# Kernel optimization log

Measured on AMD Instinct MI355X. Metric: run time of the kernel, lower is better.

## Reference

```python
import jax, jax.numpy as jnp
import numpy as np

N = 100000   # nodes
E = 3200000  # edges (before self-loops)
IN, H, OUT = 128, 256, 40

def glorot(key, shape):
    lim = (6.0 / (shape[0] + shape[1])) ** 0.5
    return jax.random.uniform(key, shape, jnp.float32, -lim, lim)

def setup_inputs() -> dict:
    key = jax.random.key(0)
    ks = jax.random.split(key, 8)
    x = jax.random.normal(ks[0], (N, IN), jnp.float32)
    edge_index = jax.random.randint(ks[1], (2, E), 0, N, dtype=jnp.int32)
    return {
        "x": x,
        "edge_index": edge_index,
        "W0": glorot(ks[2], (IN, H)),  "b0": jnp.zeros((H,), jnp.float32),
        "W1": glorot(ks[3], (H, H)),   "b1": jnp.zeros((H,), jnp.float32),
        "W2": glorot(ks[4], (H, OUT)), "b2": jnp.zeros((OUT,), jnp.float32),
    }

def _gcn_norm(edge_index, n):
    # PyG gcn_norm: add self-loops, symmetric D^{-1/2} A D^{-1/2}
    loops = jnp.arange(n, dtype=edge_index.dtype)
    src = jnp.concatenate([edge_index[0], loops])
    dst = jnp.concatenate([edge_index[1], loops])
    deg = jax.ops.segment_sum(jnp.ones_like(src, jnp.float32), dst, num_segments=n)
    dinv = jnp.where(deg > 0, jax.lax.rsqrt(deg), 0.0)
    norm = dinv[src] * dinv[dst]  # [E+N]
    return src, dst, norm

def _gcn_layer(h, W, b, src, dst, norm, n):
    h = h @ W                                   # transform first (PyG order)
    msg = h[src] * norm[:, None]                # gather + scale
    agg = jax.ops.segment_sum(msg, dst, num_segments=n)  # scatter-add
    return agg + b

def reference(x, edge_index, W0, b0, W1, b1, W2, b2):
    n = x.shape[0]
    src, dst, norm = _gcn_norm(edge_index, n)
    h = jnp.tanh(_gcn_layer(x, W0, b0, src, dst, norm, n))  # dropout = identity (eval)
    h = jnp.tanh(_gcn_layer(h, W1, b1, src, dst, norm, n))
    out = _gcn_layer(h, W2, b2, src, dst, norm, n)
    return jax.nn.log_softmax(out, axis=1)
```

## Files before the change

### kernel.cpp

```cpp
#include <hip/hip_runtime.h>
#include <hip/hip_bf16.h>
#include <cmath>


typedef unsigned short u16;
typedef __attribute__((ext_vector_type(8))) short short8;
typedef __attribute__((ext_vector_type(4))) float f32x4;

#define BSHIFT 10
#define BNODES (1 << BSHIFT)
#define ECAP   36864
#define BMASK 0x00FF00FFu

__device__ __forceinline__ u16 f2bf(float f) {
    unsigned int u = __float_as_uint(f);
    u += 0x7fffu + ((u >> 16) & 1u);
    return (u16)(u >> 16);
}

__device__ __forceinline__ int q8(float v) {
    return (int)rintf(fminf(fmaxf(v, -127.0f), 127.0f));
}


__global__ __launch_bounds__(128) void init_gcur_kernel(
        int* __restrict__ gcur, int nb) {
    int b = blockIdx.x * 128 + threadIdx.x;
    if (b < nb) gcur[b] = b * ECAP;
}

__global__ __launch_bounds__(256) void bucketize_kernel(
        const int* __restrict__ src, const int* __restrict__ dst,
        int* __restrict__ gcur, unsigned int* __restrict__ ebuf, int E) {
    __shared__ int cnt[128];
    __shared__ int base[128];
    int tid = threadIdx.x;
    int chunk0 = blockIdx.x * 8192;
    int cend = min(chunk0 + 8192, E);
    for (int r0 = chunk0; r0 < cend; r0 += 2048) {
        if (tid < 128) cnt[tid] = 0;
        __syncthreads();
        int rank[8], bk[8];
        unsigned int pk[8];
#pragma unroll
        for (int j = 0; j < 8; j++) {
            int e = r0 + j * 256 + tid;
            bk[j] = -1;
            if (e < cend) {
                int d = dst[e];
                bk[j] = d >> BSHIFT;
                pk[j] = (unsigned int)src[e] | ((unsigned int)(d & (BNODES - 1)) << 17);
                rank[j] = atomicAdd(&cnt[bk[j]], 1);
            }
        }
        __syncthreads();
        if (tid < 128 && cnt[tid] > 0) base[tid] = atomicAdd(&gcur[tid], cnt[tid]);
        __syncthreads();
#pragma unroll
        for (int j = 0; j < 8; j++)
            if (bk[j] >= 0) ebuf[base[bk[j]] + rank[j]] = pk[j];
        __syncthreads();
    }
}

__global__ __launch_bounds__(256) void bucket_csr_kernel(
        const unsigned int* __restrict__ ebuf, const int* __restrict__ gcur,
        int* __restrict__ degi, float* __restrict__ dinv,
        int* __restrict__ rs, int* __restrict__ csr, int N) {
    __shared__ int h[BNODES];
    __shared__ int lp[BNODES];
    __shared__ int ps[256];
    int b = blockIdx.x;
    int t = threadIdx.x;
    int nb0 = b << BSHIFT;
    int nodes = min(BNODES, N - nb0);

    int acc = 0;
    for (int j = t; j < b; j += 256) acc += gcur[j] - j * ECAP;
    ps[t] = acc;
    __syncthreads();
    for (int off = 128; off; off >>= 1) {
        if (t < off) ps[t] += ps[t + off];
        __syncthreads();
    }
    int bbase = ps[0];
    __syncthreads();

    for (int i = t; i < BNODES; i += 256) h[i] = 0;
    __syncthreads();
    int estart = b * ECAP;
    int eend = gcur[b];
    for (int e = estart + t; e < eend; e += 256)
        atomicAdd(&h[ebuf[e] >> 17], 1);
    __syncthreads();

    int a0 = h[t * 4], a1 = h[t * 4 + 1], a2 = h[t * 4 + 2], a3 = h[t * 4 + 3];
    int tsum = a0 + a1 + a2 + a3;
    ps[t] = tsum;
    __syncthreads();
    for (int off = 1; off < 256; off <<= 1) {
        int u = (t >= off) ? ps[t - off] : 0;
        __syncthreads();
        ps[t] += u;
        __syncthreads();
    }
    int texcl = ps[t] - tsum;
    lp[t * 4]     = texcl;
    lp[t * 4 + 1] = texcl + a0;
    lp[t * 4 + 2] = texcl + a0 + a1;
    lp[t * 4 + 3] = texcl + a0 + a1 + a2;
    __syncthreads();

    for (int i = t; i < nodes; i += 256) {
        int d = h[i];
        degi[nb0 + i] = d;
        dinv[nb0 + i] = rsqrtf((float)d + 1.0f);
        rs[nb0 + i] = bbase + lp[i];
    }
    __syncthreads();
    for (int i = t; i < BNODES; i += 256) h[i] = bbase + lp[i];
    __syncthreads();

    for (int e = estart + t; e < eend; e += 256) {
        unsigned int v = ebuf[e];
        int s = v & 0x1FFFF;
        int dl = v >> 17;
        int pos = atomicAdd(&h[dl], 1);
        csr[pos] = s;
    }
}

__global__ __launch_bounds__(256) void wt_all_kernel(
        const float* __restrict__ W0, const float* __restrict__ W1,
        const float* __restrict__ W2, u16* __restrict__ Wt0,
        u16* __restrict__ Wt1, u16* __restrict__ Wt2) {
    int i = blockIdx.x * 256 + threadIdx.x;
    if (i < 32768) {
        int k = i >> 8, c = i & 255;
        Wt0[c * 128 + k] = f2bf(W0[i]);
    } else if (i < 98304) {
        int j = i - 32768;
        int k = j >> 8, c = j & 255;
        Wt1[c * 256 + k] = f2bf(W1[j]);
    } else if (i < 108544) {
        int j = i - 98304;
        int k = j / 40, c = j - k * 40;
        Wt2[c * 256 + k] = f2bf(W2[j]);
    }
}

__global__ __launch_bounds__(256) void scale_x_kernel(
        const float* __restrict__ x, const float* __restrict__ dinv,
        unsigned int* __restrict__ out, int total4) {
    int i = blockIdx.x * 256 + threadIdx.x;
    if (i >= total4) return;
    int n = i >> 5;
    float4 v = reinterpret_cast<const float4*>(x)[i];
    float s = dinv[n] * 63.5f;
    int a0 = q8(v.x * s), a1 = q8(v.y * s), a2 = q8(v.z * s), a3 = q8(v.w * s);
    out[i] = (unsigned int)(a0 & 0xff) | ((unsigned int)(a1 & 0xff) << 8) |
             ((unsigned int)(a2 & 0xff) << 16) | ((unsigned int)(a3 & 0xff) << 24);
}

#define ACC8(q0, q1)                                                  \
    do {                                                              \
        aex += (q0) & BMASK; aox += ((q0) >> 8) & BMASK;              \
        aey += (q1) & BMASK; aoy += ((q1) >> 8) & BMASK;              \
    } while (0)

__global__ __launch_bounds__(256) void agg128_i8_kernel(
        const signed char* __restrict__ in, u16* __restrict__ out,
        const int* __restrict__ rs, const int* __restrict__ deg,
        const int* __restrict__ csr, const float* __restrict__ dinv, int n) {
    int wid = blockIdx.x * 4 + (threadIdx.x >> 6);
    if (wid >= n) return;
    int lane = threadIdx.x & 63;
    int quad = lane >> 4;
    int l16 = lane & 15;
    int start = rs[wid];
    int cnt = deg[wid];

    unsigned int aex = 0, aox = 0, aey = 0, aoy = 0;
    if (quad == 0) {
        uint2 q = *reinterpret_cast<const uint2*>(
            in + (size_t)wid * 128 + l16 * 8);
        q.x ^= 0x80808080u; q.y ^= 0x80808080u;
        ACC8(q.x, q.y);
    }
    int i = 0;
    for (; i + 16 <= cnt; i += 16) {
        int s[4];
#pragma unroll
        for (int j = 0; j < 4; j++) s[j] = csr[start + i + 4 * j + quad];
#pragma unroll
        for (int j = 0; j < 4; j++) {
            uint2 q = *reinterpret_cast<const uint2*>(
                in + (size_t)s[j] * 128 + l16 * 8);
            q.x ^= 0x80808080u; q.y ^= 0x80808080u;
            ACC8(q.x, q.y);
        }
    }
    for (; i + 4 <= cnt; i += 4) {
        int s0 = csr[start + i + quad];
        uint2 q = *reinterpret_cast<const uint2*>(
            in + (size_t)s0 * 128 + l16 * 8);
        q.x ^= 0x80808080u; q.y ^= 0x80808080u;
        ACC8(q.x, q.y);
    }
    int rem = cnt - i;
    if (quad < rem) {
        int s0 = csr[start + i + quad];
        uint2 q = *reinterpret_cast<const uint2*>(
            in + (size_t)s0 * 128 + l16 * 8);
        q.x ^= 0x80808080u; q.y ^= 0x80808080u;
        ACC8(q.x, q.y);
    }
    aex += (unsigned int)__shfl((int)aex, lane + 32);
    aox += (unsigned int)__shfl((int)aox, lane + 32);
    aey += (unsigned int)__shfl((int)aey, lane + 32);
    aoy += (unsigned int)__shfl((int)aoy, lane + 32);
    aex += (unsigned int)__shfl((int)aex, lane + 16);
    aox += (unsigned int)__shfl((int)aox, lane + 16);
    aey += (unsigned int)__shfl((int)aey, lane + 16);
    aoy += (unsigned int)__shfl((int)aoy, lane + 16);
    if (lane < 16) {
        int T = cnt + 1;
        int bias = 128 * T;
        float c = dinv[wid] * (2.0f / 127.0f);
        float f0 = (float)((int)(aex & 0xFFFFu) - bias) * c;
        float f1 = (float)((int)(aox & 0xFFFFu) - bias) * c;
        float f2 = (float)((int)(aex >> 16) - bias) * c;
        float f3 = (float)((int)(aox >> 16) - bias) * c;
        float f4 = (float)((int)(aey & 0xFFFFu) - bias) * c;
        float f5 = (float)((int)(aoy & 0xFFFFu) - bias) * c;
        float f6 = (float)((int)(aey >> 16) - bias) * c;
        float f7 = (float)((int)(aoy >> 16) - bias) * c;
        uint4 o;
        o.x = (unsigned)f2bf(f0) | ((unsigned)f2bf(f1) << 16);
        o.y = (unsigned)f2bf(f2) | ((unsigned)f2bf(f3) << 16);
        o.z = (unsigned)f2bf(f4) | ((unsigned)f2bf(f5) << 16);
        o.w = (unsigned)f2bf(f6) | ((unsigned)f2bf(f7) << 16);
        reinterpret_cast<uint4*>(out + (size_t)wid * 128)[l16] = o;
    }
}

__global__ __launch_bounds__(256) void agg_i8_kernel(
        const signed char* __restrict__ in, u16* __restrict__ out,
        const int* __restrict__ rs, const int* __restrict__ deg,
        const int* __restrict__ csr, const float* __restrict__ dinv, int n) {
    int wid = blockIdx.x * 4 + (threadIdx.x >> 6);
    if (wid >= n) return;
    int lane = threadIdx.x & 63;
    int start = rs[wid];
    int cnt = deg[wid];

    unsigned int q = *reinterpret_cast<const unsigned int*>(
        in + (size_t)wid * 256 + lane * 4) ^ 0x80808080u;
    unsigned int ae = q & BMASK, ao = (q >> 8) & BMASK;

    int i = 0;
    for (; i + 16 <= cnt; i += 16) {
        int s[16];
#pragma unroll
        for (int j = 0; j < 16; j++)
            s[j] = __builtin_amdgcn_readfirstlane(csr[start + i + j]);
        unsigned int qq[16];
#pragma unroll
        for (int j = 0; j < 16; j++)
            qq[j] = *reinterpret_cast<const unsigned int*>(
                in + (size_t)s[j] * 256 + lane * 4);
#pragma unroll
        for (int j = 0; j < 16; j++) {
            unsigned int v = qq[j] ^ 0x80808080u;
            ae += v & BMASK;
            ao += (v >> 8) & BMASK;
        }
    }
    if (i < cnt) {
        int s[16];
#pragma unroll
        for (int j = 0; j < 16; j++) {
            int e = i + j;
            e = (e < cnt) ? e : (cnt - 1);
            s[j] = __builtin_amdgcn_readfirstlane(csr[start + e]);
        }
        unsigned int qq[16];
#pragma unroll
        for (int j = 0; j < 16; j++)
            qq[j] = *reinterpret_cast<const unsigned int*>(
                in + (size_t)s[j] * 256 + lane * 4);
#pragma unroll
        for (int j = 0; j < 16; j++) {
            unsigned int m = (i + j < cnt) ? 0xFFFFFFFFu : 0u;
            unsigned int v = (qq[j] ^ 0x80808080u) & m;
            ae += v & BMASK;
            ao += (v >> 8) & BMASK;
        }
    }

    int bias = 128 * (cnt + 1);
    float c = dinv[wid] * (1.0f / 127.0f);
    float f0 = (float)((int)(ae & 0xFFFFu) - bias) * c;
    float f1 = (float)((int)(ao & 0xFFFFu) - bias) * c;
    float f2 = (float)((int)(ae >> 16) - bias) * c;
    float f3 = (float)((int)(ao >> 16) - bias) * c;
    uint2 o;
    o.x = (unsigned)f2bf(f0) | ((unsigned)f2bf(f1) << 16);
    o.y = (unsigned)f2bf(f2) | ((unsigned)f2bf(f3) << 16);
    reinterpret_cast<uint2*>(out + (size_t)wid * 256)[lane] = o;
}

template<int EPI, typename CT>
__global__ __launch_bounds__(256) void mfma_mm_kernel(
        const u16* __restrict__ A, const u16* __restrict__ Bt,
        CT* __restrict__ C, int M, int K, int NC,
        const float* __restrict__ bias, const float* __restrict__ postscale,
        float qs) {
    __shared__ u16 As[128 * 40];
    __shared__ u16 Bs[64 * 40];
    int t = threadIdx.x;
    int w = t >> 6, lane = t & 63, quad = lane >> 4, l16 = lane & 15;
    int row0 = blockIdx.x * 128;
    int col0 = blockIdx.y * 64;

    f32x4 acc[2][4];
#pragma unroll
    for (int s = 0; s < 2; s++)
#pragma unroll
        for (int nb = 0; nb < 4; nb++)
            acc[s][nb] = (f32x4){0.f, 0.f, 0.f, 0.f};

    int bn = t >> 2, bkq = (t & 3) << 3;
    for (int k0 = 0; k0 < K; k0 += 32) {
#pragma unroll
        for (int i = t; i < 512; i += 256) {
            int r = i >> 2, c = (i & 3) << 3;
            int gr = row0 + r;
            uint4 v = {0u, 0u, 0u, 0u};
            if (gr < M)
                v = *reinterpret_cast<const uint4*>(A + (size_t)gr * K + k0 + c);
            *reinterpret_cast<uint4*>(&As[r * 40 + c]) = v;
        }
        {
            int gc = col0 + bn;
            uint4 v = {0u, 0u, 0u, 0u};
            if (gc < NC)
                v = *reinterpret_cast<const uint4*>(Bt + (size_t)gc * K + k0 + bkq);
            *reinterpret_cast<uint4*>(&Bs[bn * 40 + bkq]) = v;
        }
        __syncthreads();

        short8 af[2], bf[4];
        af[0] = *reinterpret_cast<const short8*>(&As[(w * 32 + l16) * 40 + quad * 8]);
        af[1] = *reinterpret_cast<const short8*>(&As[(w * 32 + 16 + l16) * 40 + quad * 8]);
#pragma unroll
        for (int nb = 0; nb < 4; nb++)
            bf[nb] = *reinterpret_cast<const short8*>(&Bs[(nb * 16 + l16) * 40 + quad * 8]);
#pragma unroll
        for (int s = 0; s < 2; s++)
#pragma unroll
            for (int nb = 0; nb < 4; nb++)
                acc[s][nb] = __builtin_amdgcn_mfma_f32_16x16x32_bf16(
                    af[s], bf[nb], acc[s][nb], 0, 0, 0);
        __syncthreads();
    }

#pragma unroll
    for (int s = 0; s < 2; s++) {
        int rbase = row0 + w * 32 + s * 16 + quad * 4;
#pragma unroll
        for (int nb = 0; nb < 4; nb++) {
            int gc = col0 + nb * 16 + l16;
#pragma unroll
            for (int r = 0; r < 4; r++) {
                int gr = rbase + r;
                if (gr >= M || gc >= NC) continue;
                float v = acc[s][nb][r];
                if constexpr (EPI == 1) v = tanhf(v + bias[gc]);
                else                    v = v * postscale[gr];
                if constexpr (sizeof(CT) == 1) {
                    float m = qs;
                    if constexpr (EPI == 1) m *= postscale[gr];
                    C[(size_t)gr * NC + gc] = (CT)q8(v * m);
                } else {
                    C[(size_t)gr * NC + gc] = (CT)f2bf(v);
                }
            }
        }
    }
}

__global__ __launch_bounds__(256) void agg40_ls_kernel(
        const signed char* __restrict__ in, const int* __restrict__ rs,
        const int* __restrict__ deg, const int* __restrict__ csr,
        const float* __restrict__ dinv, const float* __restrict__ bias,
        float* __restrict__ out, int n) {
    int wid = blockIdx.x * 4 + (threadIdx.x >> 6);
    if (wid >= n) return;
    int lane = threadIdx.x & 63;
    int grp = lane / 5;
    int l5 = lane - grp * 5;
    bool act = lane < 60;
    int start = rs[wid];
    int cnt = deg[wid];

    unsigned int aex = 0, aox = 0, aey = 0, aoy = 0;
    if (lane < 5) {
        uint2 q = *reinterpret_cast<const uint2*>(
            in + (size_t)wid * 40 + l5 * 8);
        q.x ^= 0x80808080u; q.y ^= 0x80808080u;
        ACC8(q.x, q.y);
    }
    for (int base = 0; base < cnt; base += 12) {
        int e = base + grp;
        if (act && e < cnt) {
            int s0 = csr[start + e];
            uint2 q = *reinterpret_cast<const uint2*>(
                in + (size_t)s0 * 40 + l5 * 8);
            q.x ^= 0x80808080u; q.y ^= 0x80808080u;
            ACC8(q.x, q.y);
        }
    }
    aex += (unsigned int)__shfl((int)aex, lane + 30);
    aox += (unsigned int)__shfl((int)aox, lane + 30);
    aey += (unsigned int)__shfl((int)aey, lane + 30);
    aoy += (unsigned int)__shfl((int)aoy, lane + 30);
    aex += (unsigned int)__shfl((int)aex, lane + 15);
    aox += (unsigned int)__shfl((int)aox, lane + 15);
    aey += (unsigned int)__shfl((int)aey, lane + 15);
    aoy += (unsigned int)__shfl((int)aoy, lane + 15);
    aex += (unsigned int)__shfl((int)aex, lane + 5) + (unsigned int)__shfl((int)aex, lane + 10);
    aox += (unsigned int)__shfl((int)aox, lane + 5) + (unsigned int)__shfl((int)aox, lane + 10);
    aey += (unsigned int)__shfl((int)aey, lane + 5) + (unsigned int)__shfl((int)aey, lane + 10);
    aoy += (unsigned int)__shfl((int)aoy, lane + 5) + (unsigned int)__shfl((int)aoy, lane + 10);

    bool act5 = lane < 5;
    float s = dinv[wid];
    float v0 = -INFINITY, v1 = -INFINITY, v2 = -INFINITY, v3 = -INFINITY;
    float v4 = -INFINITY, v5 = -INFINITY, v6 = -INFINITY, v7 = -INFINITY;
    if (act5) {
        int bb = 128 * (cnt + 1);
        float c = s * (1.0f / 63.0f);
        int cc = lane * 8;
        v0 = (float)((int)(aex & 0xFFFFu) - bb) * c + bias[cc + 0];
        v1 = (float)((int)(aox & 0xFFFFu) - bb) * c + bias[cc + 1];
        v2 = (float)((int)(aex >> 16) - bb) * c + bias[cc + 2];
        v3 = (float)((int)(aox >> 16) - bb) * c + bias[cc + 3];
        v4 = (float)((int)(aey & 0xFFFFu) - bb) * c + bias[cc + 4];
        v5 = (float)((int)(aoy & 0xFFFFu) - bb) * c + bias[cc + 5];
        v6 = (float)((int)(aey >> 16) - bb) * c + bias[cc + 6];
        v7 = (float)((int)(aoy >> 16) - bb) * c + bias[cc + 7];
    }
    float m = fmaxf(fmaxf(fmaxf(v0, v1), fmaxf(v2, v3)),
                    fmaxf(fmaxf(v4, v5), fmaxf(v6, v7)));
    for (int off = 4; off; off >>= 1) m = fmaxf(m, __shfl_xor(m, off));
    float e = 0.f;
    if (act5) e = __expf(v0 - m) + __expf(v1 - m) + __expf(v2 - m) + __expf(v3 - m)
                + __expf(v4 - m) + __expf(v5 - m) + __expf(v6 - m) + __expf(v7 - m);
    for (int off = 4; off; off >>= 1) e += __shfl_xor(e, off);
    float ls = logf(e);
    if (act5) {
        float4 o0, o1;
        o0.x = v0 - m - ls; o0.y = v1 - m - ls; o0.z = v2 - m - ls; o0.w = v3 - m - ls;
        o1.x = v4 - m - ls; o1.y = v5 - m - ls; o1.z = v6 - m - ls; o1.w = v7 - m - ls;
        float4* op = reinterpret_cast<float4*>(out + (size_t)wid * 40 + lane * 8);
        op[0] = o0;
        op[1] = o1;
    }
}

extern "C" void kernel_launch(void* const* d_in, const int* in_sizes, int n_in,
                              void* d_out, int out_size, void* d_ws, size_t ws_size,
                              hipStream_t stream) {
    const float* x  = (const float*)d_in[0];
    const int*   ei = (const int*)d_in[1];
    const float* W0 = (const float*)d_in[2];
    const float* b0 = (const float*)d_in[3];
    const float* W1 = (const float*)d_in[4];
    const float* b1 = (const float*)d_in[5];
    const float* W2 = (const float*)d_in[6];
    const float* b2 = (const float*)d_in[7];
    float* out = (float*)d_out;

    const int N = in_sizes[0] / 128;
    const int E = in_sizes[1] / 2;
    const int IN = 128, H = 256, OUT = 40;
    const int NB = (N + BNODES - 1) >> BSHIFT;

    char* p = (char*)d_ws;
    auto carve = [&](size_t bytes) -> void* {
        void* r = (void*)p;
        p += (bytes + 255) & ~(size_t)255;
        return r;
    };
    float*        dinv = (float*)carve((size_t)N * 4);
    int*          degi = (int*)  carve((size_t)N * 4);
    int*          rs   = (int*)  carve((size_t)N * 4);
    int*          gcur = (int*)  carve((size_t)128 * 4);
    int*          csr  = (int*)  carve((size_t)E * 4);
    unsigned int* ebuf = (unsigned int*)carve((size_t)NB * ECAP * 4);
    u16*          Wt0  = (u16*)  carve((size_t)IN * H * 2);
    u16*          Wt1  = (u16*)  carve((size_t)H * H * 2);
    u16*          Wt2  = (u16*)  carve((size_t)H * OUT * 2);
    u16*          U1   = (u16*)  carve((size_t)N * H * 2);
    u16*          U2   = (u16*)  carve((size_t)N * H * 2);

    signed char* Xq   = (signed char*)U1;
    u16*         T0bf = U1 + (size_t)N * IN / 2 + 64;
    signed char* H0q  = (signed char*)U2;
    u16*         T1bf = U1;
    u16*         h1bf = U2;
    signed char* G2q  = (signed char*)U1;

    const int* src = ei;
    const int* dst = ei + E;

    int gW = (N + 3) / 4;
    int gMM = (N + 127) / 128;
    int gA = (E + 8191) / 8192;

    init_gcur_kernel<<<1, 128, 0, stream>>>(gcur, NB);
    bucketize_kernel<<<gA, 256, 0, stream>>>(src, dst, gcur, ebuf, E);
    bucket_csr_kernel<<<NB, 256, 0, stream>>>(
        ebuf, gcur, degi, dinv, rs, csr, N);

    wt_all_kernel<<<(108544 + 255) / 256, 256, 0, stream>>>(
        W0, W1, W2, Wt0, Wt1, Wt2);

    int t4x = N * (IN / 4);
    scale_x_kernel<<<(t4x + 255) / 256, 256, 0, stream>>>(
        x, dinv, (unsigned int*)Xq, t4x);
    agg128_i8_kernel<<<gW, 256, 0, stream>>>(Xq, T0bf, rs, degi, csr, dinv, N);
    mfma_mm_kernel<1, signed char><<<dim3(gMM, H / 64), 256, 0, stream>>>(
        T0bf, Wt0, H0q, N, IN, H, b0, dinv, 127.0f);

    agg_i8_kernel<<<gW, 256, 0, stream>>>(H0q, T1bf, rs, degi, csr, dinv, N);
    mfma_mm_kernel<1, u16><<<dim3(gMM, H / 64), 256, 0, stream>>>(
        T1bf, Wt1, h1bf, N, H, H, b1, nullptr, 0.f);

    mfma_mm_kernel<0, signed char><<<dim3(gMM, 1), 256, 0, stream>>>(
        h1bf, Wt2, G2q, N, H, OUT, nullptr, dinv, 63.0f);
    agg40_ls_kernel<<<gW, 256, 0, stream>>>(G2q, rs, degi, csr, dinv, b2, out, N);
}
```

Before: 605.5 us.

## Quantize layer-1 output to int8 and pad layer-2 features to 64-byte rows

Layer 1's tanh output is now stored as int8 instead of bf16. A new dedicated MFMA kernel consumes it, dequantizing int8 to bf16 in shared memory and computing the 40-column projection, then writes int8 rows padded to a 64-byte stride. The final aggregation/log-softmax kernel is reworked to use 4 lanes x 16 bytes per edge with 16 edges per iteration and power-of-two shuffle reductions, replacing the awkward 5-lane grouping. This cuts the memory traffic of the intermediate activation and aligns gathers, at the cost of extra quantization error and padded storage.

```diff
diff --git a/kernel.cpp b/kernel.cpp
--- a/kernel.cpp
+++ b/kernel.cpp
@@ -380,11 +380,93 @@
                 else                    v = v * postscale[gr];
                 if constexpr (sizeof(CT) == 1) {
                     float m = qs;
-                    if constexpr (EPI == 1) m *= postscale[gr];
+                    if constexpr (EPI == 1) { if (postscale) m *= postscale[gr]; }
                     C[(size_t)gr * NC + gc] = (CT)q8(v * m);
                 } else {
                     C[(size_t)gr * NC + gc] = (CT)f2bf(v);
                 }
+            }
+        }
+    }
+}
+
+__global__ __launch_bounds__(256) void mfma_mm2_i8_kernel(
+        const signed char* __restrict__ A, const u16* __restrict__ Bt,
+        signed char* __restrict__ C, int M, const float* __restrict__ postscale) {
+    __shared__ u16 As[128 * 40];
+    __shared__ u16 Bs[48 * 40];
+    int t = threadIdx.x;
+    int w = t >> 6, lane = t & 63, quad = lane >> 4, l16 = lane & 15;
+    int row0 = blockIdx.x * 128;
+
+    f32x4 acc[2][3];
+#pragma unroll
+    for (int s = 0; s < 2; s++)
+#pragma unroll
+        for (int nb = 0; nb < 3; nb++)
+            acc[s][nb] = (f32x4){0.f, 0.f, 0.f, 0.f};
+
+    int ar = t >> 1, aoff = (t & 1) << 4;
+    for (int k0 = 0; k0 < 256; k0 += 32) {
+        {
+            int gr = row0 + ar;
+            uint4 v = {0u, 0u, 0u, 0u};
+            if (gr < M)
+                v = *reinterpret_cast<const uint4*>(A + (size_t)gr * 256 + k0 + aoff);
+            unsigned int wds[8];
+#pragma unroll
+            for (int u = 0; u < 4; u++) {
+                unsigned int q = (&v.x)[u];
+                float g0 = (float)(int)(signed char)(q & 0xffu);
+                float g1 = (float)(int)(signed char)((q >> 8) & 0xffu);
+                float g2 = (float)(int)(signed char)((q >> 16) & 0xffu);
+                float g3 = (float)(int)(signed char)(q >> 24);
+                wds[u * 2]     = (unsigned)f2bf(g0) | ((unsigned)f2bf(g1) << 16);
+                wds[u * 2 + 1] = (unsigned)f2bf(g2) | ((unsigned)f2bf(g3) << 16);
+            }
+            uint4 o0 = {wds[0], wds[1], wds[2], wds[3]};
+            uint4 o1 = {wds[4], wds[5], wds[6], wds[7]};
+            *reinterpret_cast<uint4*>(&As[ar * 40 + aoff]) = o0;
+            *reinterpret_cast<uint4*>(&As[ar * 40 + aoff + 8]) = o1;
+        }
+        if (t < 192) {
+            int gc = t >> 2, kq = (t & 3) << 3;
+            uint4 v = {0u, 0u, 0u, 0u};
+            if (gc < 40)
+                v = *reinterpret_cast<const uint4*>(Bt + (size_t)gc * 256 + k0 + kq);
+            *reinterpret_cast<uint4*>(&Bs[gc * 40 + kq]) = v;
+        }
+        __syncthreads();
+
+        short8 af[2], bf[3];
+        af[0] = *reinterpret_cast<const short8*>(&As[(w * 32 + l16) * 40 + quad * 8]);
+        af[1] = *reinterpret_cast<const short8*>(&As[(w * 32 + 16 + l16) * 40 + quad * 8]);
+#pragma unroll
+        for (int nb = 0; nb < 3; nb++)
+            bf[nb] = *reinterpret_cast<const short8*>(&Bs[(nb * 16 + l16) * 40 + quad * 8]);
+#pragma unroll
+        for (int s = 0; s < 2; s++)
+#pragma unroll
+            for (int nb = 0; nb < 3; nb++)
+                acc[s][nb] = __builtin_amdgcn_mfma_f32_16x16x32_bf16(
+                    af[s], bf[nb], acc[s][nb], 0, 0, 0);
+        __syncthreads();
+    }
+
+    const float QS = 63.0f / 127.0f;
+#pragma unroll
+    for (int s = 0; s < 2; s++) {
+        int rbase = row0 + w * 32 + s * 16 + quad * 4;
+#pragma unroll
+        for (int nb = 0; nb < 3; nb++) {
+            int gc = nb * 16 + l16;
+            if (gc >= 40) continue;
+#pragma unroll
+            for (int r = 0; r < 4; r++) {
+                int gr = rbase + r;
+                if (gr >= M) continue;
+                float v = acc[s][nb][r] * postscale[gr] * QS;
+                C[(size_t)gr * 64 + gc] = (signed char)q8(v);
             }
         }
     }
@@ -398,74 +480,79 @@
     int wid = blockIdx.x * 4 + (threadIdx.x >> 6);
     if (wid >= n) return;
     int lane = threadIdx.x & 63;
-    int grp = lane / 5;
-    int l5 = lane - grp * 5;
-    bool act = lane < 60;
+    int grp = lane >> 2;
+    int l4 = lane & 3;
     int start = rs[wid];
     int cnt = deg[wid];
 
-    unsigned int aex = 0, aox = 0, aey = 0, aoy = 0;
-    if (lane < 5) {
-        uint2 q = *reinterpret_cast<const uint2*>(
-            in + (size_t)wid * 40 + l5 * 8);
-        q.x ^= 0x80808080u; q.y ^= 0x80808080u;
-        ACC8(q.x, q.y);
-    }
-    for (int base = 0; base < cnt; base += 12) {
+    unsigned int a0 = 0, a1 = 0, a2 = 0, a3 = 0, a4 = 0, a5 = 0, a6 = 0, a7 = 0;
+#define ACCR(q)                                                        \
+    do {                                                               \
+        unsigned int x = (q).x ^ 0x80808080u, y = (q).y ^ 0x80808080u, \
+                     z = (q).z ^ 0x80808080u, w = (q).w ^ 0x80808080u; \
+        a0 += x & BMASK; a1 += (x >> 8) & BMASK;                       \
+        a2 += y & BMASK; a3 += (y >> 8) & BMASK;                       \
+        a4 += z & BMASK; a5 += (z >> 8) & BMASK;                       \
+        a6 += w & BMASK; a7 += (w >> 8) & BMASK;                       \
+    } while (0)
+
+    if (grp == 0) {
+        uint4 q = *reinterpret_cast<const uint4*>(in + (size_t)wid * 64 + l4 * 16);
+        ACCR(q);
+    }
+    for (int base = 0; base < cnt; base += 16) {
         int e = base + grp;
-        if (act && e < cnt) {
+        if (e < cnt) {
             int s0 = csr[start + e];
-            uint2 q = *reinterpret_cast<const uint2*>(
-                in + (size_t)s0 * 40 + l5 * 8);
-            q.x ^= 0x80808080u; q.y ^= 0x80808080u;
-            ACC8(q.x, q.y);
-        }
-    }
-    aex += (unsigned int)__shfl((int)aex, lane + 30);
-    aox += (unsigned int)__shfl((int)aox, lane + 30);
-    aey += (unsigned int)__shfl((int)aey, lane + 30);
-    aoy += (unsigned int)__shfl((int)aoy, lane + 30);
-    aex += (unsigned int)__shfl((int)aex, lane + 15);
-    aox += (unsigned int)__shfl((int)aox, lane + 15);
-    aey += (unsigned int)__shfl((int)aey, lane + 15);
-    aoy += (unsigned int)__shfl((int)aoy, lane + 15);
-    aex += (unsigned int)__shfl((int)aex, lane + 5) + (unsigned int)__shfl((int)aex, lane + 10);
-    aox += (unsigned int)__shfl((int)aox, lane + 5) + (unsigned int)__shfl((int)aox, lane + 10);
-    aey += (unsigned int)__shfl((int)aey, lane + 5) + (unsigned int)__shfl((int)aey, lane + 10);
-    aoy += (unsigned int)__shfl((int)aoy, lane + 5) + (unsigned int)__shfl((int)aoy, lane + 10);
-
-    bool act5 = lane < 5;
-    float s = dinv[wid];
-    float v0 = -INFINITY, v1 = -INFINITY, v2 = -INFINITY, v3 = -INFINITY;
-    float v4 = -INFINITY, v5 = -INFINITY, v6 = -INFINITY, v7 = -INFINITY;
-    if (act5) {
+            uint4 q = *reinterpret_cast<const uint4*>(in + (size_t)s0 * 64 + l4 * 16);
+            ACCR(q);
+        }
+    }
+#undef ACCR
+#define MRG(a)                                              \
+    a += (unsigned int)__shfl((int)(a), lane + 32);         \
+    a += (unsigned int)__shfl((int)(a), lane + 16);         \
+    a += (unsigned int)__shfl((int)(a), lane + 8);          \
+    a += (unsigned int)__shfl((int)(a), lane + 4);
+    MRG(a0) MRG(a1) MRG(a2) MRG(a3) MRG(a4) MRG(a5) MRG(a6) MRG(a7)
+#undef MRG
+
+    if (lane < 4) {
         int bb = 128 * (cnt + 1);
-        float c = s * (1.0f / 63.0f);
-        int cc = lane * 8;
-        v0 = (float)((int)(aex & 0xFFFFu) - bb) * c + bias[cc + 0];
-        v1 = (float)((int)(aox & 0xFFFFu) - bb) * c + bias[cc + 1];
-        v2 = (float)((int)(aex >> 16) - bb) * c + bias[cc + 2];
-        v3 = (float)((int)(aox >> 16) - bb) * c + bias[cc + 3];
-        v4 = (float)((int)(aey & 0xFFFFu) - bb) * c + bias[cc + 4];
-        v5 = (float)((int)(aoy & 0xFFFFu) - bb) * c + bias[cc + 5];
-        v6 = (float)((int)(aey >> 16) - bb) * c + bias[cc + 6];
-        v7 = (float)((int)(aoy >> 16) - bb) * c + bias[cc + 7];
-    }
-    float m = fmaxf(fmaxf(fmaxf(v0, v1), fmaxf(v2, v3)),
-                    fmaxf(fmaxf(v4, v5), fmaxf(v6, v7)));
-    for (int off = 4; off; off >>= 1) m = fmaxf(m, __shfl_xor(m, off));
-    float e = 0.f;
-    if (act5) e = __expf(v0 - m) + __expf(v1 - m) + __expf(v2 - m) + __expf(v3 - m)
-                + __expf(v4 - m) + __expf(v5 - m) + __expf(v6 - m) + __expf(v7 - m);
-    for (int off = 4; off; off >>= 1) e += __shfl_xor(e, off);
-    float ls = logf(e);
-    if (act5) {
-        float4 o0, o1;
-        o0.x = v0 - m - ls; o0.y = v1 - m - ls; o0.z = v2 - m - ls; o0.w = v3 - m - ls;
-        o1.x = v4 - m - ls; o1.y = v5 - m - ls; o1.z = v6 - m - ls; o1.w = v7 - m - ls;
-        float4* op = reinterpret_cast<float4*>(out + (size_t)wid * 40 + lane * 8);
-        op[0] = o0;
-        op[1] = o1;
+        float c = dinv[wid] * (1.0f / 63.0f);
+        int cbase = lane * 16;
+        unsigned int ae[4] = {a0, a2, a4, a6};
+        unsigned int ao[4] = {a1, a3, a5, a7};
+        float v[16];
+#pragma unroll
+        for (int u = 0; u < 4; u++) {
+            int cb = cbase + u * 4;
+            v[u*4+0] = (cb+0 < 40) ? ((int)(ae[u] & 0xFFFFu) - bb) * c + bias[cb+0] : -INFINITY;
+            v[u*4+1] = (cb+1 < 40) ? ((int)(ao[u] & 0xFFFFu) - bb) * c + bias[cb+1] : -INFINITY;
+            v[u*4+2] = (cb+2 < 40) ? ((int)(ae[u] >> 16)     - bb) * c + bias[cb+2] : -INFINITY;
+            v[u*4+3] = (cb+3 < 40) ? ((int)(ao[u] >> 16)     - bb) * c + bias[cb+3] : -INFINITY;
+        }
+        float m = -INFINITY;
+#pragma unroll
+        for (int j = 0; j < 16; j++) m = fmaxf(m, v[j]);
+        m = fmaxf(m, __shfl_xor(m, 1));
+        m = fmaxf(m, __shfl_xor(m, 2));
+        float e = 0.f;
+#pragma unroll
+        for (int j = 0; j < 16; j++) e += (v[j] > -INFINITY) ? __expf(v[j] - m) : 0.f;
+        e += __shfl_xor(e, 1);
+        e += __shfl_xor(e, 2);
+        float ls = logf(e);
+#pragma unroll
+        for (int k = 0; k < 4; k++) {
+            int cb = cbase + k * 4;
+            if (cb < 40) {
+                float4 o;
+                o.x = v[k*4+0] - m - ls; o.y = v[k*4+1] - m - ls;
+                o.z = v[k*4+2] - m - ls; o.w = v[k*4+3] - m - ls;
+                *reinterpret_cast<float4*>(out + (size_t)wid * 40 + cb) = o;
+            }
+        }
     }
 }
 
@@ -509,7 +596,7 @@
     u16*         T0bf = U1 + (size_t)N * IN / 2 + 64;
     signed char* H0q  = (signed char*)U2;
     u16*         T1bf = U1;
-    u16*         h1bf = U2;
+    signed char* h1q  = (signed char*)U2;
     signed char* G2q  = (signed char*)U1;
 
     const int* src = ei;
@@ -535,10 +622,9 @@
         T0bf, Wt0, H0q, N, IN, H, b0, dinv, 127.0f);
 
     agg_i8_kernel<<<gW, 256, 0, stream>>>(H0q, T1bf, rs, degi, csr, dinv, N);
-    mfma_mm_kernel<1, u16><<<dim3(gMM, H / 64), 256, 0, stream>>>(
-        T1bf, Wt1, h1bf, N, H, H, b1, nullptr, 0.f);
-
-    mfma_mm_kernel<0, signed char><<<dim3(gMM, 1), 256, 0, stream>>>(
-        h1bf, Wt2, G2q, N, H, OUT, nullptr, dinv, 63.0f);
+    mfma_mm_kernel<1, signed char><<<dim3(gMM, H / 64), 256, 0, stream>>>(
+        T1bf, Wt1, h1q, N, H, H, b1, nullptr, 127.0f);
+
+    mfma_mm2_i8_kernel<<<gMM, 256, 0, stream>>>(h1q, Wt2, G2q, N, dinv);
     agg40_ls_kernel<<<gW, 256, 0, stream>>>(G2q, rs, degi, csr, dinv, b2, out, N);
 }
```

Result: slower. 647.5 us (+6.9%).
